# Kernel tuning notes

Measured on AMD Instinct MI355X. Metric: run time of the kernel, lower is better.

## Reference

```python
import jax, jax.numpy as jnp
import numpy as np

B, N, C, M = 64, 8732, 21, 16  # batch, priors (SSD300), classes (VOC), max objects


def setup_inputs() -> dict:
    key = jax.random.key(0)
    k1, k2 = jax.random.split(key)
    confOut = jax.random.normal(k1, (B, N, C), dtype=jnp.float32)
    bboxOut = jax.random.normal(k2, (B, N, 4), dtype=jnp.float32)

    rng = np.random.default_rng(0)
    # prior boxes [x1,y1,x2,y2], positive width/height
    px1 = rng.uniform(0.0, 0.8, (N, 1)).astype(np.float32)
    py1 = rng.uniform(0.0, 0.8, (N, 1)).astype(np.float32)
    pw = rng.uniform(0.05, 0.2, (N, 1)).astype(np.float32)
    ph = rng.uniform(0.05, 0.2, (N, 1)).astype(np.float32)
    predBoxes = np.concatenate([px1, py1, px1 + pw, py1 + ph], axis=1)

    # target layout: [num, (cls,x1,y1,x2,y2,k) * M]
    target = np.zeros((B, 1 + 6 * M), dtype=np.float32)
    target[:, 0] = rng.integers(1, M + 1, B)
    cls = rng.integers(1, C, (B, M)).astype(np.float32)  # all positive classes
    tx1 = rng.uniform(0.0, 0.8, (B, M)).astype(np.float32)
    ty1 = rng.uniform(0.0, 0.8, (B, M)).astype(np.float32)
    tw = rng.uniform(0.05, 0.2, (B, M)).astype(np.float32)
    th = rng.uniform(0.05, 0.2, (B, M)).astype(np.float32)
    ks = np.stack([rng.choice(N, M, replace=False) for _ in range(B)]).astype(np.float32)
    flat = np.stack([cls, tx1, ty1, tx1 + tw, ty1 + th, ks], axis=-1).reshape(B, 6 * M)
    target[:, 1:] = flat

    return {"confOut": confOut, "bboxOut": bboxOut,
            "target": jnp.asarray(target), "predBoxes": jnp.asarray(predBoxes)}


def _encode_box(true_box, pred_box):
    # standard SSD center/size encoding: (tc-pc)/pw, log(tw/pw)
    tcx = (true_box[..., 0] + true_box[..., 2]) * 0.5
    tcy = (true_box[..., 1] + true_box[..., 3]) * 0.5
    tw = true_box[..., 2] - true_box[..., 0]
    th = true_box[..., 3] - true_box[..., 1]
    pcx = (pred_box[..., 0] + pred_box[..., 2]) * 0.5
    pcy = (pred_box[..., 1] + pred_box[..., 3]) * 0.5
    pw = pred_box[..., 2] - pred_box[..., 0]
    ph = pred_box[..., 3] - pred_box[..., 1]
    return jnp.stack([(tcx - pcx) / pw, (tcy - pcy) / ph,
                      jnp.log(tw / pw), jnp.log(th / ph)], axis=-1)


def _ssd_loss(confOut, bboxOut, target, predBoxes):
    b, n, c = confOut.shape
    m = (target.shape[1] - 1) // 6
    t = target[:, 1:1 + 6 * m].reshape(b, m, 6)
    cls = t[..., 0].astype(jnp.int32)          # [B,M]
    tbox = t[..., 1:5]                          # [B,M,4]
    k = t[..., 5].astype(jnp.int32)             # [B,M] prior index
    num = target[:, 0].astype(jnp.int32)        # [B]
    valid = jnp.arange(m)[None, :] < num[:, None]      # [B,M]
    pos = valid & (cls > 0)
    bi = jnp.broadcast_to(jnp.arange(b)[:, None], (b, m))

    # ---- conf target assignment (scatter per object onto prior grid) ----
    posmask = jnp.zeros((b, n), bool).at[bi, k].max(pos)
    assigned = jnp.zeros((b, n), bool).at[bi, k].max(valid)  # score zeroed for all assigned
    conf_cls = jnp.zeros((b, n), jnp.int32).at[bi, k].max(jnp.where(pos, cls, 0))
    pnum = jnp.sum(pos)

    # ---- hard negative mining: globally sort bg log-prob ascending ----
    logp = jax.nn.log_softmax(confOut, axis=-1)             # [B,N,C]
    bg = jnp.where(assigned, 0.0, logp[..., 0]).reshape(-1)  # assigned -> 0 (sorts last)
    order = jnp.argsort(bg)
    pos_sorted = posmask.reshape(-1)[order]
    hit_pos = jnp.cumsum(pos_sorted.astype(jnp.int32)) > 0   # early-break emulation
    sel_sorted = (jnp.arange(b * n) < 3 * pnum) & (~hit_pos)
    negmask = jnp.zeros(b * n, bool).at[order].set(sel_sorted).reshape(b, n)

    selmask = posmask | negmask
    ce = -jnp.take_along_axis(logp, conf_cls[..., None], axis=-1)[..., 0]  # [B,N]
    conf_loss = jnp.sum(jnp.where(selmask, ce, 0.0)) / jnp.maximum(jnp.sum(selmask), 1)

    # ---- bbox target assignment + SmoothL1 on positives ----
    ebox = _encode_box(tbox, predBoxes[k])                   # [B,M,4]
    btgt = jnp.zeros((b, n, 4)).at[bi, k].add(jnp.where(valid[..., None], ebox, 0.0))
    bmask = jnp.zeros((b, n), bool).at[bi, k].max(valid)
    d = bboxOut - btgt
    ad = jnp.abs(d)
    sl1 = jnp.where(ad < 1.0, 0.5 * d * d, ad - 0.5)
    denom = jnp.maximum(jnp.sum(bmask) * 4, 1)
    bbox_loss = jnp.sum(jnp.where(bmask[..., None], sl1, 0.0)) / denom
    return conf_loss, bbox_loss


def reference(confOut, bboxOut, target, predBoxes):
    return _ssd_loss(confOut, bboxOut, target, predBoxes)
```

## Files before the change

kernel.cpp:

```cpp
#include <hip/hip_runtime.h>

constexpr int B = 64, N = 8732, C = 21, M = 16;
constexpr int TROW = 1 + 6 * M;
constexpr int NBIN = 2048;
constexpr unsigned BASE16 = 15103u;
constexpr int NSLAB = 8;
constexpr int TILE = 256;
constexpr int NTILES = (N + TILE - 1) / TILE;
constexpr int BPB = 8;
constexpr float FSCALE = 262144.0f;
constexpr unsigned long long CNT1 = 1ull << 44;
constexpr unsigned long long FIXMASK = (1ull << 44) - 1;

typedef __attribute__((address_space(1))) const unsigned int g_as_t;
typedef __attribute__((address_space(3))) unsigned int l_as_t;

__device__ __forceinline__ unsigned f2key(float f) {
  unsigned u = __float_as_uint(f);
  return (u & 0x80000000u) ? ~u : (u | 0x80000000u);
}
__device__ __forceinline__ float key2f(unsigned k) {
  unsigned u = (k & 0x80000000u) ? (k ^ 0x80000000u) : ~k;
  return __uint_as_float(u);
}

__global__ __launch_bounds__(256) void k_zero(unsigned long long* __restrict__ z) {
  int idx = blockIdx.x * 256 + threadIdx.x;
  z[idx] = 0ull;
}

__global__ __launch_bounds__(256) void k_logp(
    const float* __restrict__ conf, const float* __restrict__ bbox,
    const float* __restrict__ target, const float* __restrict__ pred,
    unsigned long long* __restrict__ slab1, float4* __restrict__ batchCtl) {
  __shared__ __align__(16) float sbuf[2][TILE * C];
  __shared__ unsigned long long shist[NBIN];
  __shared__ int sk[M];
  int b = blockIdx.y, bx = blockIdx.x, tid = threadIdx.x;
  int wave = tid >> 6, lane = tid & 63;

  for (int i = tid; i < NBIN; i += 256) shist[i] = 0ull;
  const float* tr = target + (size_t)b * TROW;
  if (tid < M) {
    int num = (int)tr[0];
    sk[tid] = (tid < num) ? (int)tr[1 + 6 * tid + 5] : -1;
  }

  const size_t cbase = (size_t)b * N;
  int nt = (NTILES - 1 - bx) / BPB + 1;

#define STAGE(kt, bi)                                                       \
  {                                                                         \
    int tt_ = bx + (kt) * BPB;                                              \
    int n0_ = tt_ * TILE;                                                   \
    int rows_ = min(TILE, N - n0_);                                         \
    int bytes_ = rows_ * C * 4;             \
    const char* gb_ = (const char*)(conf + (cbase + n0_) * C);              \
    char* lb_ = (char*)sbuf[bi];                                            \
    for (int c_ = wave; c_ * 1024 < bytes_; c_ += 4) {                      \
      int off_ = c_ * 1024 + lane * 16;                                     \
      if (off_ + 16 <= bytes_) {                                            \
        __builtin_amdgcn_global_load_lds((g_as_t*)(gb_ + off_),             \
                                         (l_as_t*)(lb_ + c_ * 1024),        \
                                         16, 0, 0);                         \
      }                                                                     \
    }                                                                       \
  }

  STAGE(0, 0);
  __syncthreads();

  for (int t = 0; t < nt; ++t) {
    if (t + 1 < nt) STAGE(t + 1, (t + 1) & 1);
    {
      int tt_ = bx + t * BPB;
      int n0_ = tt_ * TILE;
      int rows_ = min(TILE, N - n0_);
      if (tid < rows_) {
        int n = n0_ + tid;
        const float* x = sbuf[t & 1] + tid * C;
        float s0 = __expf(x[0]) + __expf(x[4]) + __expf(x[8]) + __expf(x[12]) + __expf(x[16]);
        float s1 = __expf(x[1]) + __expf(x[5]) + __expf(x[9]) + __expf(x[13]) + __expf(x[17]);
        float s2 = __expf(x[2]) + __expf(x[6]) + __expf(x[10]) + __expf(x[14]) + __expf(x[18]);
        float s3 = __expf(x[3]) + __expf(x[7]) + __expf(x[11]) + __expf(x[15]) + __expf(x[19]);
        float s = (s0 + s1) + (s2 + s3) + __expf(x[20]);
        float lp = x[0] - __logf(s);
        bool asg = false;
        for (int j = 0; j < M; j++) asg |= (sk[j] == n);
        if (!asg) {
          int idx = ((int)(f2key(lp) >> 16) - (int)BASE16) >> 1;
          idx = min(max(idx, 0), NBIN - 1);
          atomicAdd(&shist[idx],
                    CNT1 | (unsigned long long)((-lp) * FSCALE + 0.5f));
        }
      }
    }
    __syncthreads();
  }
#undef STAGE

  unsigned long long* sg = slab1 + (size_t)(bx & (NSLAB - 1)) * NBIN;
  for (int i = tid; i < NBIN; i += 256) {
    unsigned long long v = shist[i];
    if (v) atomicAdd(&sg[i], v);
  }

  if (bx == 0) {
    float myValid = 0.f, myPos = 0.f, myCE = 0.f, mySL = 0.f;
    if (tid < M && sk[tid] >= 0) {
      const float* e = tr + 1 + 6 * tid;
      int cls = (int)e[0];
      float tx1 = e[1], ty1 = e[2], tx2 = e[3], ty2 = e[4];
      int k = sk[tid];
      float p0 = pred[k * 4 + 0], p1 = pred[k * 4 + 1];
      float p2 = pred[k * 4 + 2], p3 = pred[k * 4 + 3];
      float pw = p2 - p0, ph = p3 - p1;
      float pcx = (p0 + p2) * 0.5f, pcy = (p1 + p3) * 0.5f;
      float tw = tx2 - tx1, th = ty2 - ty1;
      float tcx = (tx1 + tx2) * 0.5f, tcy = (ty1 + ty2) * 0.5f;
      float ebv[4];
      ebv[0] = (tcx - pcx) / pw;
      ebv[1] = (tcy - pcy) / ph;
      ebv[2] = __logf(tw / pw);
      ebv[3] = __logf(th / ph);
      const float* bo = bbox + ((size_t)b * N + k) * 4;
      float sl = 0.f;
      for (int j = 0; j < 4; j++) {
        float d = bo[j] - ebv[j];
        float ad = fabsf(d);
        sl += (ad < 1.f) ? 0.5f * d * d : ad - 0.5f;
      }
      myValid = 1.f; mySL = sl;
      if (cls > 0) {
        const float* x = conf + ((size_t)b * N + k) * C;
        float s = 0.f;
        for (int c = 0; c < C; c++) s += __expf(x[c]);
        float lp = x[cls] - __logf(s);
        myPos = 1.f; myCE = -lp;
      }
    }
    if (tid < 64) {
      for (int off = 32; off; off >>= 1) {
        myValid += __shfl_down(myValid, off, 64);
        myPos   += __shfl_down(myPos, off, 64);
        myCE    += __shfl_down(myCE, off, 64);
        mySL    += __shfl_down(mySL, off, 64);
      }
      if (tid == 0) batchCtl[b] = make_float4(myPos, myValid, myCE, mySL);
    }
  }
}

__global__ __launch_bounds__(1024) void k_fin(
    const unsigned long long* __restrict__ slab1,
    const float4* __restrict__ batchCtl, float* __restrict__ out) {
  __shared__ unsigned long long sm[NBIN];
  __shared__ unsigned long long sscan[1024];
  __shared__ unsigned srank;
  __shared__ float sp, sva, sce, ssl;
  __shared__ double sNeg;
  int tid = threadIdx.x;

  if (tid < 64) {
    float4 v = batchCtl[tid];
    float p = v.x, va = v.y, ce = v.z, sl = v.w;
    for (int off = 32; off; off >>= 1) {
      p  += __shfl_down(p, off, 64);
      va += __shfl_down(va, off, 64);
      ce += __shfl_down(ce, off, 64);
      sl += __shfl_down(sl, off, 64);
    }
    if (tid == 0) {
      sp = p; sva = va; sce = ce; ssl = sl;
      srank = 3u * (unsigned)(p + 0.5f);
      sNeg = 0.0;
    }
  }

  for (int k = 0; k < NBIN / 1024; k++) {
    int bin = tid + k * 1024;
    unsigned long long v = 0ull;
    for (int s = 0; s < NSLAB; s++) v += slab1[(size_t)s * NBIN + bin];
    sm[bin] = v;
  }
  __syncthreads();

  unsigned long long h2[2];
  unsigned long long part = 0ull;
  for (int j = 0; j < 2; j++) { h2[j] = sm[tid * 2 + j]; part += h2[j]; }
  sscan[tid] = part;
  __syncthreads();
  for (int off = 1; off < 1024; off <<= 1) {
    unsigned long long add = (tid >= off) ? sscan[tid - off] : 0ull;
    __syncthreads();
    sscan[tid] += add;
    __syncthreads();
  }

  unsigned rank = srank;
  if (rank) {
    unsigned long long cum = sscan[tid] - part;
    for (int j = 0; j < 2; j++) {
      unsigned long long h = h2[j];
      unsigned c0 = (unsigned)(cum >> 44);
      unsigned c1 = (unsigned)((cum + h) >> 44);
      if (c0 < rank && c1 >= rank) {
        unsigned t = (unsigned)(tid * 2 + j);
        unsigned r = rank - c0;
        unsigned long long fixBelow = cum & FIXMASK;
        float ceEdge = -key2f((BASE16 + 2u * t) << 16);
        sNeg = (double)fixBelow / 262144.0 + (double)r * (double)ceEdge;
      }
      cum += h;
    }
  }
  __syncthreads();
  if (tid == 0) {
    out[0] = (sce + (float)sNeg) / fmaxf(4.0f * sp, 1.0f);
    out[1] = ssl / fmaxf(4.0f * sva, 1.0f);
  }
}

extern "C" void kernel_launch(void* const* d_in, const int* in_sizes, int n_in,
                              void* d_out, int out_size, void* d_ws, size_t ws_size,
                              hipStream_t stream) {
  const float* conf = (const float*)d_in[0];
  const float* bbox = (const float*)d_in[1];
  const float* target = (const float*)d_in[2];
  const float* pred = (const float*)d_in[3];
  float* out = (float*)d_out;

  char* ws = (char*)d_ws;
  unsigned long long* slab1 = (unsigned long long*)ws;
  size_t off = (size_t)NSLAB * NBIN * 8;
  float4* batchCtl = (float4*)(ws + off); off += 64 * 16;

  k_zero<<<64, 256, 0, stream>>>(slab1);
  k_logp<<<dim3(BPB, B), 256, 0, stream>>>(conf, bbox, target, pred,
                                           slab1, batchCtl);
  k_fin<<<1, 1024, 0, stream>>>(slab1, batchCtl, out);
}
```

Measured before the change: 28.43 us.

## Single-buffer LDS tile via register copy and double blocks per batch

```diff
diff --git a/kernel.cpp b/kernel.cpp
--- a/kernel.cpp
+++ b/kernel.cpp
@@ -7,7 +7,7 @@
 constexpr int NSLAB = 8;
 constexpr int TILE = 256;
 constexpr int NTILES = (N + TILE - 1) / TILE;
-constexpr int BPB = 8;
+constexpr int BPB = 16;
 constexpr float FSCALE = 262144.0f;
 constexpr unsigned long long CNT1 = 1ull << 44;
 constexpr unsigned long long FIXMASK = (1ull << 44) - 1;
@@ -33,7 +33,7 @@
     const float* __restrict__ conf, const float* __restrict__ bbox,
     const float* __restrict__ target, const float* __restrict__ pred,
     unsigned long long* __restrict__ slab1, float4* __restrict__ batchCtl) {
-  __shared__ __align__(16) float sbuf[2][TILE * C];
+  __shared__ __align__(16) float sbuf[TILE * C];
   __shared__ unsigned long long shist[NBIN];
   __shared__ int sk[M];
   int b = blockIdx.y, bx = blockIdx.x, tid = threadIdx.x;
@@ -49,14 +49,14 @@
   const size_t cbase = (size_t)b * N;
   int nt = (NTILES - 1 - bx) / BPB + 1;
 
-#define STAGE(kt, bi)                                                       \
+#define STAGE(kt)                                                           \
   {                                                                         \
     int tt_ = bx + (kt) * BPB;                                              \
     int n0_ = tt_ * TILE;                                                   \
     int rows_ = min(TILE, N - n0_);                                         \
-    int bytes_ = rows_ * C * 4;             \
+    int bytes_ = rows_ * C * 4;              \
     const char* gb_ = (const char*)(conf + (cbase + n0_) * C);              \
-    char* lb_ = (char*)sbuf[bi];                                            \
+    char* lb_ = (char*)sbuf;                                                \
     for (int c_ = wave; c_ * 1024 < bytes_; c_ += 4) {                      \
       int off_ = c_ * 1024 + lane * 16;                                     \
       if (off_ + 16 <= bytes_) {                                            \
@@ -67,32 +67,36 @@
     }                                                                       \
   }
 
-  STAGE(0, 0);
+  STAGE(0);
   __syncthreads();
 
   for (int t = 0; t < nt; ++t) {
-    if (t + 1 < nt) STAGE(t + 1, (t + 1) & 1);
-    {
-      int tt_ = bx + t * BPB;
-      int n0_ = tt_ * TILE;
-      int rows_ = min(TILE, N - n0_);
-      if (tid < rows_) {
-        int n = n0_ + tid;
-        const float* x = sbuf[t & 1] + tid * C;
-        float s0 = __expf(x[0]) + __expf(x[4]) + __expf(x[8]) + __expf(x[12]) + __expf(x[16]);
-        float s1 = __expf(x[1]) + __expf(x[5]) + __expf(x[9]) + __expf(x[13]) + __expf(x[17]);
-        float s2 = __expf(x[2]) + __expf(x[6]) + __expf(x[10]) + __expf(x[14]) + __expf(x[18]);
-        float s3 = __expf(x[3]) + __expf(x[7]) + __expf(x[11]) + __expf(x[15]) + __expf(x[19]);
-        float s = (s0 + s1) + (s2 + s3) + __expf(x[20]);
-        float lp = x[0] - __logf(s);
-        bool asg = false;
-        for (int j = 0; j < M; j++) asg |= (sk[j] == n);
-        if (!asg) {
-          int idx = ((int)(f2key(lp) >> 16) - (int)BASE16) >> 1;
-          idx = min(max(idx, 0), NBIN - 1);
-          atomicAdd(&shist[idx],
-                    CNT1 | (unsigned long long)((-lp) * FSCALE + 0.5f));
-        }
+    int tt_ = bx + t * BPB;
+    int n0_ = tt_ * TILE;
+    int rows_ = min(TILE, N - n0_);
+    float r[C];
+    if (tid < rows_) {
+      const float* x = sbuf + tid * C;
+      #pragma unroll
+      for (int c = 0; c < C; c++) r[c] = x[c];
+    }
+    __syncthreads();
+    if (t + 1 < nt) STAGE(t + 1);
+    if (tid < rows_) {
+      int n = n0_ + tid;
+      float s0 = __expf(r[0]) + __expf(r[4]) + __expf(r[8]) + __expf(r[12]) + __expf(r[16]);
+      float s1 = __expf(r[1]) + __expf(r[5]) + __expf(r[9]) + __expf(r[13]) + __expf(r[17]);
+      float s2 = __expf(r[2]) + __expf(r[6]) + __expf(r[10]) + __expf(r[14]) + __expf(r[18]);
+      float s3 = __expf(r[3]) + __expf(r[7]) + __expf(r[11]) + __expf(r[15]) + __expf(r[19]);
+      float s = (s0 + s1) + (s2 + s3) + __expf(r[20]);
+      float lp = r[0] - __logf(s);
+      bool asg = false;
+      for (int j = 0; j < M; j++) asg |= (sk[j] == n);
+      if (!asg) {
+        int idx = ((int)(f2key(lp) >> 16) - (int)BASE16) >> 1;
+        idx = min(max(idx, 0), NBIN - 1);
+        atomicAdd(&shist[idx],
+                  CNT1 | (unsigned long long)((-lp) * FSCALE + 0.5f));
       }
     }
     __syncthreads();
```

After: 32.99 us. +16.1%, slower.

## Triple-buffer conf tile staging with partial vmcnt barriers and halve histogram bins

Applied to the files above, without the earlier changes.

```diff
diff --git a/kernel.cpp b/kernel.cpp
--- a/kernel.cpp
+++ b/kernel.cpp
@@ -2,7 +2,7 @@
 
 constexpr int B = 64, N = 8732, C = 21, M = 16;
 constexpr int TROW = 1 + 6 * M;
-constexpr int NBIN = 2048;
+constexpr int NBIN = 1024;
 constexpr unsigned BASE16 = 15103u;
 constexpr int NSLAB = 8;
 constexpr int TILE = 256;
@@ -24,6 +24,19 @@
   return __uint_as_float(u);
 }
 
+__device__ __forceinline__ void pipe_barrier_vm5() {
+  asm volatile("s_waitcnt vmcnt(5) lgkmcnt(0)" ::: "memory");
+  __builtin_amdgcn_sched_barrier(0);
+  __builtin_amdgcn_s_barrier();
+  __builtin_amdgcn_sched_barrier(0);
+}
+__device__ __forceinline__ void pipe_barrier_vm0() {
+  asm volatile("s_waitcnt vmcnt(0) lgkmcnt(0)" ::: "memory");
+  __builtin_amdgcn_sched_barrier(0);
+  __builtin_amdgcn_s_barrier();
+  __builtin_amdgcn_sched_barrier(0);
+}
+
 __global__ __launch_bounds__(256) void k_zero(unsigned long long* __restrict__ z) {
   int idx = blockIdx.x * 256 + threadIdx.x;
   z[idx] = 0ull;
@@ -33,7 +46,7 @@
     const float* __restrict__ conf, const float* __restrict__ bbox,
     const float* __restrict__ target, const float* __restrict__ pred,
     unsigned long long* __restrict__ slab1, float4* __restrict__ batchCtl) {
-  __shared__ __align__(16) float sbuf[2][TILE * C];
+  __shared__ __align__(16) float sbuf[3][TILE * C];
   __shared__ unsigned long long shist[NBIN];
   __shared__ int sk[M];
   int b = blockIdx.y, bx = blockIdx.x, tid = threadIdx.x;
@@ -54,7 +67,7 @@
     int tt_ = bx + (kt) * BPB;                                              \
     int n0_ = tt_ * TILE;                                                   \
     int rows_ = min(TILE, N - n0_);                                         \
-    int bytes_ = rows_ * C * 4;             \
+    int bytes_ = rows_ * C * 4;              \
     const char* gb_ = (const char*)(conf + (cbase + n0_) * C);              \
     char* lb_ = (char*)sbuf[bi];                                            \
     for (int c_ = wave; c_ * 1024 < bytes_; c_ += 4) {                      \
@@ -68,17 +81,18 @@
   }
 
   STAGE(0, 0);
-  __syncthreads();
+  STAGE(1, 1);
+  pipe_barrier_vm5();
 
   for (int t = 0; t < nt; ++t) {
-    if (t + 1 < nt) STAGE(t + 1, (t + 1) & 1);
+    if (t + 2 < nt) STAGE(t + 2, (t + 2) % 3);
     {
       int tt_ = bx + t * BPB;
       int n0_ = tt_ * TILE;
       int rows_ = min(TILE, N - n0_);
       if (tid < rows_) {
         int n = n0_ + tid;
-        const float* x = sbuf[t & 1] + tid * C;
+        const float* x = sbuf[t % 3] + tid * C;
         float s0 = __expf(x[0]) + __expf(x[4]) + __expf(x[8]) + __expf(x[12]) + __expf(x[16]);
         float s1 = __expf(x[1]) + __expf(x[5]) + __expf(x[9]) + __expf(x[13]) + __expf(x[17]);
         float s2 = __expf(x[2]) + __expf(x[6]) + __expf(x[10]) + __expf(x[14]) + __expf(x[18]);
@@ -88,16 +102,21 @@
         bool asg = false;
         for (int j = 0; j < M; j++) asg |= (sk[j] == n);
         if (!asg) {
-          int idx = ((int)(f2key(lp) >> 16) - (int)BASE16) >> 1;
+          int idx = ((int)(f2key(lp) >> 16) - (int)BASE16) >> 2;
           idx = min(max(idx, 0), NBIN - 1);
           atomicAdd(&shist[idx],
                     CNT1 | (unsigned long long)((-lp) * FSCALE + 0.5f));
         }
       }
     }
-    __syncthreads();
+    if (t + 1 < nt) {
+      if (t + 2 < nt) pipe_barrier_vm5();
+      else            pipe_barrier_vm0();
+    }
   }
 #undef STAGE
+
+  __syncthreads();
 
   unsigned long long* sg = slab1 + (size_t)(bx & (NSLAB - 1)) * NBIN;
   for (int i = tid; i < NBIN; i += 256) {
@@ -154,7 +173,6 @@
 __global__ __launch_bounds__(1024) void k_fin(
     const unsigned long long* __restrict__ slab1,
     const float4* __restrict__ batchCtl, float* __restrict__ out) {
-  __shared__ unsigned long long sm[NBIN];
   __shared__ unsigned long long sscan[1024];
   __shared__ unsigned srank;
   __shared__ float sp, sva, sce, ssl;
@@ -177,18 +195,9 @@
     }
   }
 
-  for (int k = 0; k < NBIN / 1024; k++) {
-    int bin = tid + k * 1024;
-    unsigned long long v = 0ull;
-    for (int s = 0; s < NSLAB; s++) v += slab1[(size_t)s * NBIN + bin];
-    sm[bin] = v;
-  }
-  __syncthreads();
-
-  unsigned long long h2[2];
-  unsigned long long part = 0ull;
-  for (int j = 0; j < 2; j++) { h2[j] = sm[tid * 2 + j]; part += h2[j]; }
-  sscan[tid] = part;
+  unsigned long long hv = 0ull;
+  for (int s = 0; s < NSLAB; s++) hv += slab1[(size_t)s * NBIN + tid];
+  sscan[tid] = hv;
   __syncthreads();
   for (int off = 1; off < 1024; off <<= 1) {
     unsigned long long add = (tid >= off) ? sscan[tid - off] : 0ull;
@@ -199,19 +208,14 @@
 
   unsigned rank = srank;
   if (rank) {
-    unsigned long long cum = sscan[tid] - part;
-    for (int j = 0; j < 2; j++) {
-      unsigned long long h = h2[j];
-      unsigned c0 = (unsigned)(cum >> 44);
-      unsigned c1 = (unsigned)((cum + h) >> 44);
-      if (c0 < rank && c1 >= rank) {
-        unsigned t = (unsigned)(tid * 2 + j);
-        unsigned r = rank - c0;
-        unsigned long long fixBelow = cum & FIXMASK;
-        float ceEdge = -key2f((BASE16 + 2u * t) << 16);
-        sNeg = (double)fixBelow / 262144.0 + (double)r * (double)ceEdge;
-      }
-      cum += h;
+    unsigned long long cum = sscan[tid] - hv;
+    unsigned c0 = (unsigned)(cum >> 44);
+    unsigned c1 = (unsigned)((cum + hv) >> 44);
+    if (c0 < rank && c1 >= rank) {
+      unsigned r = rank - c0;
+      unsigned long long fixBelow = cum & FIXMASK;
+      float ceEdge = -key2f((BASE16 + 4u * (unsigned)tid) << 16);
+      sNeg = (double)fixBelow / 262144.0 + (double)r * (double)ceEdge;
     }
   }
   __syncthreads();
@@ -235,7 +239,7 @@
   size_t off = (size_t)NSLAB * NBIN * 8;
   float4* batchCtl = (float4*)(ws + off); off += 64 * 16;
 
-  k_zero<<<64, 256, 0, stream>>>(slab1);
+  k_zero<<<32, 256, 0, stream>>>(slab1);
   k_logp<<<dim3(BPB, B), 256, 0, stream>>>(conf, bbox, target, pred,
                                            slab1, batchCtl);
   k_fin<<<1, 1024, 0, stream>>>(slab1, batchCtl, out);
```

Measured after the change: 26.66 us. 6.2% less time.
